# Performance work log

Hardware: AMD Instinct MI355X
Metric: run time of the kernel (lower is better)

The kernel has to match this reference:

```python
import jax, jax.numpy as jnp
import numpy as np

B, C, H, W = 4, 64, 64, 64
CQK = C // 4  # query/key channels = in_dim // 4


def setup_inputs() -> dict:
    key = jax.random.key(0)
    ks = jax.random.split(key, 9)
    s = 0.05
    return {
        "x": jax.random.normal(ks[0], (B, C, H, W), jnp.float32),
        "x_RGB": jax.random.normal(ks[1], (B, C, H, W), jnp.float32),
        "Wq": jax.random.normal(ks[2], (CQK, C), jnp.float32) * s,  # 1x1 conv weight
        "bq": jax.random.normal(ks[3], (CQK,), jnp.float32) * s,
        "Wk": jax.random.normal(ks[4], (CQK, C), jnp.float32) * s,
        "bk": jax.random.normal(ks[5], (CQK,), jnp.float32) * s,
        "Wv": jax.random.normal(ks[6], (C, C), jnp.float32) * s,
        "bv": jax.random.normal(ks[7], (C,), jnp.float32) * s,
        "lam": jnp.zeros((1,), jnp.float32) + 0.5,  # nn.Parameter init is 0; use 0.5 so output depends on attention
    }


def reference(x, x_RGB, Wq, bq, Wk, bk, Wv, bv, lam):
    b, c, h, w = x.shape
    n = h * w
    xf = x.reshape(b, c, n)          # B,C,N
    xr = x_RGB.reshape(b, c, n)      # B,C,N
    # 1x1 convs are channel matmuls
    q = jnp.einsum('oc,bcn->bno', Wq, xr) + bq            # B,N,Cqk  (permuted query)
    k = jnp.einsum('oc,bcn->bon', Wk, xf) + bk[:, None]   # B,Cqk,N
    v = jnp.einsum('oc,bcn->bon', Wv, xf) + bv[:, None]   # B,C,N
    energy = jnp.einsum('bio,boj->bij', q, k)             # B,N,N
    attention = jax.nn.softmax(energy, axis=-1)
    # out[b,c,i] = sum_j V[b,c,j] * attention[b,i,j]
    out = jnp.einsum('bcj,bij->bci', v, attention)        # B,C,N
    out = out.reshape(b, c, h, w)
    return lam[0] * out + x
```

## Files before the change

### kernel.cpp

```cpp
#include <hip/hip_runtime.h>
#include <hip/hip_bf16.h>
#include <math.h>

#define B_   4
#define C_   64
#define N_   4096
#define L2E  1.4426950408889634f

typedef __attribute__((ext_vector_type(8)))  short bf16x8;
typedef __attribute__((ext_vector_type(4)))  float f32x4;
typedef __attribute__((ext_vector_type(16))) float f32x16;
typedef __attribute__((ext_vector_type(4)))  uint  uint4v;

#define MFMA16(a,b,c) __builtin_amdgcn_mfma_f32_16x16x32_bf16(a,b,c,0,0,0)
#define MFMA32(a,b,c) __builtin_amdgcn_mfma_f32_32x32x16_bf16(a,b,c,0,0,0)

static __device__ inline uint cvtpk(float lo, float hi) {
    uint r;
    asm("v_cvt_pk_bf16_f32 %0, %1, %2" : "=v"(r) : "v"(lo), "v"(hi));
    return r;
}
static __device__ inline void plswap(uint &a, uint &b) {
    asm("v_permlane32_swap_b32 %0, %1" : "+v"(a), "+v"(b));
}
static __device__ inline float ex2(float x) {
#if __has_builtin(__builtin_amdgcn_exp2f)
    return __builtin_amdgcn_exp2f(x);
#else
    return exp2f(x);
#endif
}
static __device__ inline float frcp(float x) {
#if __has_builtin(__builtin_amdgcn_rcpf)
    return __builtin_amdgcn_rcpf(x);
#else
    return 1.0f / x;
#endif
}
static __device__ inline float tsum16(const f32x16 &s) {
    float a0 = s[0] + s[1],  a1 = s[2] + s[3];
    float a2 = s[4] + s[5],  a3 = s[6] + s[7];
    float a4 = s[8] + s[9],  a5 = s[10] + s[11];
    float a6 = s[12] + s[13], a7 = s[14] + s[15];
    a0 += a1; a2 += a3; a4 += a5; a6 += a7;
    return (a0 + a2) + (a4 + a6);
}
static __device__ inline bf16x8 pk8(float f0, float f1, float f2, float f3,
                                    float f4, float f5, float f6, float f7) {
    uint4v u = {cvtpk(f0, f1), cvtpk(f2, f3), cvtpk(f4, f5), cvtpk(f6, f7)};
    return __builtin_bit_cast(bf16x8, u);
}

__global__ __launch_bounds__(256) void qkv_mfma(
    const float* __restrict__ x, const float* __restrict__ xrgb,
    const float* __restrict__ Wq, const float* __restrict__ bq,
    const float* __restrict__ Wk, const float* __restrict__ bk,
    const float* __restrict__ Wv, const float* __restrict__ bv,
    ushort* __restrict__ Qo, ushort* __restrict__ Ko, ushort* __restrict__ Vo)
{
    const int t = threadIdx.x, b = blockIdx.y, n0 = blockIdx.x * 32;
    const int w = t >> 6, lane = t & 63, li = lane & 15, g = lane >> 4;
    const int pw = w & 1, oh = w >> 1;

    const int px = n0 + pw * 16 + li;

    bf16x8 bxf[2], brf[2];
    #pragma unroll
    for (int kk = 0; kk < 2; ++kk) {
        const int c0 = kk * 32 + g * 8;
        const float* xb = x + ((size_t)b * C_ + c0) * N_ + px;
        float fx[8];
        #pragma unroll
        for (int r = 0; r < 8; ++r) fx[r] = xb[(size_t)r * N_];
        bxf[kk] = pk8(fx[0], fx[1], fx[2], fx[3], fx[4], fx[5], fx[6], fx[7]);
        if (oh == 0) {
            const float* rb = xrgb + ((size_t)b * C_ + c0) * N_ + px;
            float fr[8];
            #pragma unroll
            for (int r = 0; r < 8; ++r) fr[r] = rb[(size_t)r * N_];
            brf[kk] = pk8(fr[0], fr[1], fr[2], fr[3], fr[4], fr[5], fr[6], fr[7]);
        } else {
            brf[kk] = bxf[kk];
        }
    }

    const f32x4 cz = {0.f, 0.f, 0.f, 0.f};
    #pragma unroll
    for (int j = 0; j < 3; ++j) {
        const int ot = oh * 3 + j;
        const float* wsrc;
        const float* bsrc;
        if (ot == 0)      { wsrc = Wq + li * 64;                   bsrc = bq; }
        else if (ot == 1) { wsrc = Wk + li * 64;                   bsrc = bk; }
        else              { wsrc = Wv + ((ot - 2) * 16 + li) * 64; bsrc = bv + (ot - 2) * 16; }
        const float s = (ot == 0) ? L2E : 1.0f;

        f32x4 acc = cz;
        #pragma unroll
        for (int kk = 0; kk < 2; ++kk) {
            const int c0 = kk * 32 + g * 8;
            const float4 a  = *(const float4*)(wsrc + c0);
            const float4 c4 = *(const float4*)(wsrc + c0 + 4);
            const bf16x8 wa = pk8(a.x * s, a.y * s, a.z * s, a.w * s,
                                  c4.x * s, c4.y * s, c4.z * s, c4.w * s);
            acc = MFMA16(wa, (ot == 0 ? brf[kk] : bxf[kk]), acc);
        }
        const float b0 = bsrc[g * 4 + 0] * s, b1 = bsrc[g * 4 + 1] * s;
        const float b2 = bsrc[g * 4 + 2] * s, b3 = bsrc[g * 4 + 3] * s;
        if (ot < 2) {
            uint2 pwd;
            pwd.x = cvtpk(acc[0] + b0, acc[1] + b1);
            pwd.y = cvtpk(acc[2] + b2, acc[3] + b3);
            ushort* dst = (ot == 0 ? Qo : Ko) + (size_t)(b * N_ + px) * 16 + g * 4;
            *(uint2*)dst = pwd;
        } else {
            const size_t base = (((size_t)b * (N_ / 16) + (px >> 4)) * 64
                                 + (ot - 2) * 16 + g * 4) * 16 + (px & 15);
            const uint v01 = cvtpk(acc[0] + b0, acc[1] + b1);
            const uint v23 = cvtpk(acc[2] + b2, acc[3] + b3);
            Vo[base]      = (ushort)(v01 & 0xffff);
            Vo[base + 16] = (ushort)(v01 >> 16);
            Vo[base + 32] = (ushort)(v23 & 0xffff);
            Vo[base + 48] = (ushort)(v23 >> 16);
        }
    }
}

__global__ __launch_bounds__(1024, 4) void flash32(
    const ushort* __restrict__ Qg, const ushort* __restrict__ Kg,
    const ushort* __restrict__ VT, const float* __restrict__ x,
    const float* __restrict__ lam, float* __restrict__ out)
{
    __shared__ float OT[16][64][33];
    __shared__ float LC[16][33];

    const int t = threadIdx.x, w = t >> 6, lane = t & 63;
    const int l31 = lane & 31, h = lane >> 5;
    const int qh = w & 1, jg = w >> 1;

    const int wg = blockIdx.x;
    const int b  = wg >> 6;
    const int i0 = (wg & 63) * 64;

    const bf16x8 qf = *(const bf16x8*)(Qg + ((size_t)(b * N_ + i0 + qh * 32 + l31)) * 16 + h * 8);

    const size_t jbase = (size_t)jg * 512;
    const ushort* kp = Kg + ((size_t)(b * N_) + jbase + l31) * 16 + h * 8;
    const ushort* vt = VT + (((size_t)b * (N_ / 16) + jg * 32) * 64 + l31) * 16 + h * 8;

    f32x16 a0, a1, z16;
    #pragma unroll
    for (int i = 0; i < 16; ++i) { a0[i] = 0.f; a1[i] = 0.f; z16[i] = 0.f; }
    float lsum = 0.f;

    #pragma unroll 1
    for (int jt = 0; jt < 16; ++jt) {
        const bf16x8 kf = *(const bf16x8*)(kp + (size_t)jt * 512);

        f32x16 st = MFMA32(kf, qf, z16);
        #pragma unroll
        for (int i = 0; i < 16; ++i) st[i] = ex2(st[i]);
        lsum += tsum16(st);

        uint A0 = cvtpk(st[0],  st[1]),  A1 = cvtpk(st[2],  st[3]);
        uint B0 = cvtpk(st[4],  st[5]),  B1 = cvtpk(st[6],  st[7]);
        uint C0 = cvtpk(st[8],  st[9]),  C1 = cvtpk(st[10], st[11]);
        uint D0 = cvtpk(st[12], st[13]), D1 = cvtpk(st[14], st[15]);
        plswap(A0, B0); plswap(A1, B1); plswap(C0, D0); plswap(C1, D1);
        uint4v u0 = {A0, A1, B0, B1}, u1 = {C0, C1, D0, D1};
        const bf16x8 pf0 = __builtin_bit_cast(bf16x8, u0);
        const bf16x8 pf1 = __builtin_bit_cast(bf16x8, u1);

        const ushort* vtj = vt + (size_t)jt * 2048;
        {
            const bf16x8 va = *(const bf16x8*)(vtj);
            const bf16x8 vb = *(const bf16x8*)(vtj + 512);
            a0 = MFMA32(va, pf0, a0);
            a1 = MFMA32(vb, pf0, a1);
        }
        {
            const bf16x8 va = *(const bf16x8*)(vtj + 1024);
            const bf16x8 vb = *(const bf16x8*)(vtj + 1536);
            a0 = MFMA32(va, pf1, a0);
            a1 = MFMA32(vb, pf1, a1);
        }
    }

    lsum += __shfl_xor(lsum, 32);
    if (h == 0) LC[w][l31] = lsum;

    #pragma unroll
    for (int r = 0; r < 16; ++r) {
        const int c = (r & 3) + 8 * (r >> 2) + 4 * h;
        OT[w][c][l31]      = a0[r];
        OT[w][c + 32][l31] = a1[r];
    }
    __syncthreads();

    {
        const int qh2 = t >> 9, c = (t >> 3) & 63, q0 = (t & 7) * 4;
        const float la = lam[0];
        f32x4 o = {0.f, 0.f, 0.f, 0.f};
        f32x4 ls = {0.f, 0.f, 0.f, 0.f};
        #pragma unroll
        for (int p = 0; p < 8; ++p) {
            const int idx = p * 2 + qh2;
            const f32x4 v = *(const f32x4*)&OT[idx][c][q0];
            o[0] += v[0]; o[1] += v[1]; o[2] += v[2]; o[3] += v[3];
            #pragma unroll
            for (int k = 0; k < 4; ++k) ls[k] += LC[idx][q0 + k];
        }
        const size_t off = ((size_t)b * C_ + c) * N_ + i0 + qh2 * 32 + q0;
        const float4 xv = *(const float4*)(x + off);
        float4 res;
        res.x = la * o[0] * frcp(ls[0]) + xv.x;
        res.y = la * o[1] * frcp(ls[1]) + xv.y;
        res.z = la * o[2] * frcp(ls[2]) + xv.z;
        res.w = la * o[3] * frcp(ls[3]) + xv.w;
        *(float4*)(out + off) = res;
    }
}

extern "C" void kernel_launch(void* const* d_in, const int* in_sizes, int n_in,
                              void* d_out, int out_size, void* d_ws, size_t ws_size,
                              hipStream_t stream)
{
    (void)in_sizes; (void)n_in; (void)out_size; (void)ws_size;
    const float* x    = (const float*)d_in[0];
    const float* xrgb = (const float*)d_in[1];
    const float* Wq   = (const float*)d_in[2];
    const float* bq   = (const float*)d_in[3];
    const float* Wk   = (const float*)d_in[4];
    const float* bk   = (const float*)d_in[5];
    const float* Wv   = (const float*)d_in[6];
    const float* bv   = (const float*)d_in[7];
    const float* lam  = (const float*)d_in[8];
    float* out = (float*)d_out;

    ushort* Qw = (ushort*)d_ws;
    ushort* Kw = Qw + (size_t)B_ * N_ * 16;
    ushort* Vw = Kw + (size_t)B_ * N_ * 16;

    qkv_mfma<<<dim3(N_ / 32, B_), 256, 0, stream>>>(
        x, xrgb, Wq, bq, Wk, bk, Wv, bv, Qw, Kw, Vw);

    flash32<<<dim3(256), 1024, 0, stream>>>(
        Qw, Kw, Vw, x, lam, out);
}
```

Before: 30.53 us.

## Process both query halves per wave to reuse K/V loads across queries

Measured after the change: 32.58 us. +6.7%, slower.

```diff
diff --git a/kernel.cpp b/kernel.cpp
--- a/kernel.cpp
+++ b/kernel.cpp
@@ -49,6 +49,16 @@
                                     float f4, float f5, float f6, float f7) {
     uint4v u = {cvtpk(f0, f1), cvtpk(f2, f3), cvtpk(f4, f5), cvtpk(f6, f7)};
     return __builtin_bit_cast(bf16x8, u);
+}
+static __device__ inline void pack_p(const f32x16 &st, bf16x8 &pf0, bf16x8 &pf1) {
+    uint A0 = cvtpk(st[0],  st[1]),  A1 = cvtpk(st[2],  st[3]);
+    uint B0 = cvtpk(st[4],  st[5]),  B1 = cvtpk(st[6],  st[7]);
+    uint C0 = cvtpk(st[8],  st[9]),  C1 = cvtpk(st[10], st[11]);
+    uint D0 = cvtpk(st[12], st[13]), D1 = cvtpk(st[14], st[15]);
+    plswap(A0, B0); plswap(A1, B1); plswap(C0, D0); plswap(C1, D1);
+    uint4v u0 = {A0, A1, B0, B1}, u1 = {C0, C1, D0, D1};
+    pf0 = __builtin_bit_cast(bf16x8, u0);
+    pf1 = __builtin_bit_cast(bf16x8, u1);
 }
 
 __global__ __launch_bounds__(256) void qkv_mfma(
@@ -61,7 +71,6 @@
     const int t = threadIdx.x, b = blockIdx.y, n0 = blockIdx.x * 32;
     const int w = t >> 6, lane = t & 63, li = lane & 15, g = lane >> 4;
     const int pw = w & 1, oh = w >> 1;
-
     const int px = n0 + pw * 16 + li;
 
     bf16x8 bxf[2], brf[2];
@@ -132,92 +141,115 @@
     const float* __restrict__ lam, float* __restrict__ out)
 {
     __shared__ float OT[16][64][33];
-    __shared__ float LC[16][33];
+    __shared__ float LC[2][16][33];
 
     const int t = threadIdx.x, w = t >> 6, lane = t & 63;
     const int l31 = lane & 31, h = lane >> 5;
-    const int qh = w & 1, jg = w >> 1;
 
     const int wg = blockIdx.x;
     const int b  = wg >> 6;
     const int i0 = (wg & 63) * 64;
 
-    const bf16x8 qf = *(const bf16x8*)(Qg + ((size_t)(b * N_ + i0 + qh * 32 + l31)) * 16 + h * 8);
-
-    const size_t jbase = (size_t)jg * 512;
+    const bf16x8 qfA = *(const bf16x8*)(Qg + ((size_t)(b * N_ + i0 + l31)) * 16 + h * 8);
+    const bf16x8 qfB = *(const bf16x8*)(Qg + ((size_t)(b * N_ + i0 + 32 + l31)) * 16 + h * 8);
+
+    const size_t jbase = (size_t)w * 256;
     const ushort* kp = Kg + ((size_t)(b * N_) + jbase + l31) * 16 + h * 8;
-    const ushort* vt = VT + (((size_t)b * (N_ / 16) + jg * 32) * 64 + l31) * 16 + h * 8;
-
-    f32x16 a0, a1, z16;
-    #pragma unroll
-    for (int i = 0; i < 16; ++i) { a0[i] = 0.f; a1[i] = 0.f; z16[i] = 0.f; }
-    float lsum = 0.f;
+    const ushort* vt = VT + (((size_t)b * (N_ / 16) + w * 16) * 64 + l31) * 16 + h * 8;
+
+    f32x16 aA0, aA1, aB0, aB1, z16;
+    #pragma unroll
+    for (int i = 0; i < 16; ++i) {
+        aA0[i] = 0.f; aA1[i] = 0.f; aB0[i] = 0.f; aB1[i] = 0.f; z16[i] = 0.f;
+    }
+    float lA = 0.f, lB = 0.f;
 
     #pragma unroll 1
-    for (int jt = 0; jt < 16; ++jt) {
+    for (int jt = 0; jt < 8; ++jt) {
         const bf16x8 kf = *(const bf16x8*)(kp + (size_t)jt * 512);
-
-        f32x16 st = MFMA32(kf, qf, z16);
-        #pragma unroll
-        for (int i = 0; i < 16; ++i) st[i] = ex2(st[i]);
-        lsum += tsum16(st);
-
-        uint A0 = cvtpk(st[0],  st[1]),  A1 = cvtpk(st[2],  st[3]);
-        uint B0 = cvtpk(st[4],  st[5]),  B1 = cvtpk(st[6],  st[7]);
-        uint C0 = cvtpk(st[8],  st[9]),  C1 = cvtpk(st[10], st[11]);
-        uint D0 = cvtpk(st[12], st[13]), D1 = cvtpk(st[14], st[15]);
-        plswap(A0, B0); plswap(A1, B1); plswap(C0, D0); plswap(C1, D1);
-        uint4v u0 = {A0, A1, B0, B1}, u1 = {C0, C1, D0, D1};
-        const bf16x8 pf0 = __builtin_bit_cast(bf16x8, u0);
-        const bf16x8 pf1 = __builtin_bit_cast(bf16x8, u1);
-
         const ushort* vtj = vt + (size_t)jt * 2048;
+        const bf16x8 va0 = *(const bf16x8*)(vtj);
+        const bf16x8 vb0 = *(const bf16x8*)(vtj + 512);
+        const bf16x8 va1 = *(const bf16x8*)(vtj + 1024);
+        const bf16x8 vb1 = *(const bf16x8*)(vtj + 1536);
+
         {
-            const bf16x8 va = *(const bf16x8*)(vtj);
-            const bf16x8 vb = *(const bf16x8*)(vtj + 512);
-            a0 = MFMA32(va, pf0, a0);
-            a1 = MFMA32(vb, pf0, a1);
+            f32x16 st = MFMA32(kf, qfA, z16);
+            #pragma unroll
+            for (int i = 0; i < 16; ++i) st[i] = ex2(st[i]);
+            lA += tsum16(st);
+            bf16x8 pf0, pf1;
+            pack_p(st, pf0, pf1);
+            aA0 = MFMA32(va0, pf0, aA0);
+            aA1 = MFMA32(vb0, pf0, aA1);
+            aA0 = MFMA32(va1, pf1, aA0);
+            aA1 = MFMA32(vb1, pf1, aA1);
         }
         {
-            const bf16x8 va = *(const bf16x8*)(vtj + 1024);
-            const bf16x8 vb = *(const bf16x8*)(vtj + 1536);
-            a0 = MFMA32(va, pf1, a0);
-            a1 = MFMA32(vb, pf1, a1);
-        }
-    }
-
-    lsum += __shfl_xor(lsum, 32);
-    if (h == 0) LC[w][l31] = lsum;
+            f32x16 st = MFMA32(kf, qfB, z16);
+            #pragma unroll
+            for (int i = 0; i < 16; ++i) st[i] = ex2(st[i]);
+            lB += tsum16(st);
+            bf16x8 pf0, pf1;
+            pack_p(st, pf0, pf1);
+            aB0 = MFMA32(va0, pf0, aB0);
+            aB1 = MFMA32(vb0, pf0, aB1);
+            aB0 = MFMA32(va1, pf1, aB0);
+            aB1 = MFMA32(vb1, pf1, aB1);
+        }
+    }
+
+    lA += __shfl_xor(lA, 32);
+    lB += __shfl_xor(lB, 32);
+    if (h == 0) { LC[0][w][l31] = lA; LC[1][w][l31] = lB; }
+
+    const float la = lam[0];
 
     #pragma unroll
     for (int r = 0; r < 16; ++r) {
         const int c = (r & 3) + 8 * (r >> 2) + 4 * h;
-        OT[w][c][l31]      = a0[r];
-        OT[w][c + 32][l31] = a1[r];
+        OT[w][c][l31]      = aA0[r];
+        OT[w][c + 32][l31] = aA1[r];
     }
     __syncthreads();
-
     {
-        const int qh2 = t >> 9, c = (t >> 3) & 63, q0 = (t & 7) * 4;
-        const float la = lam[0];
-        f32x4 o = {0.f, 0.f, 0.f, 0.f};
-        f32x4 ls = {0.f, 0.f, 0.f, 0.f};
-        #pragma unroll
-        for (int p = 0; p < 8; ++p) {
-            const int idx = p * 2 + qh2;
-            const f32x4 v = *(const f32x4*)&OT[idx][c][q0];
-            o[0] += v[0]; o[1] += v[1]; o[2] += v[2]; o[3] += v[3];
-            #pragma unroll
-            for (int k = 0; k < 4; ++k) ls[k] += LC[idx][q0 + k];
-        }
-        const size_t off = ((size_t)b * C_ + c) * N_ + i0 + qh2 * 32 + q0;
-        const float4 xv = *(const float4*)(x + off);
-        float4 res;
-        res.x = la * o[0] * frcp(ls[0]) + xv.x;
-        res.y = la * o[1] * frcp(ls[1]) + xv.y;
-        res.z = la * o[2] * frcp(ls[2]) + xv.z;
-        res.w = la * o[3] * frcp(ls[3]) + xv.w;
-        *(float4*)(out + off) = res;
+        const int c = t >> 4, qd = (t & 15) * 2;
+        float o0 = 0.f, o1 = 0.f, l0 = 0.f, l1 = 0.f;
+        #pragma unroll
+        for (int p = 0; p < 16; ++p) {
+            o0 += OT[p][c][qd];     o1 += OT[p][c][qd + 1];
+            l0 += LC[0][p][qd];     l1 += LC[0][p][qd + 1];
+        }
+        const size_t off = ((size_t)b * C_ + c) * N_ + i0 + qd;
+        const float2 xv = *(const float2*)(x + off);
+        float2 res;
+        res.x = la * o0 * frcp(l0) + xv.x;
+        res.y = la * o1 * frcp(l1) + xv.y;
+        *(float2*)(out + off) = res;
+    }
+    __syncthreads();
+
+    #pragma unroll
+    for (int r = 0; r < 16; ++r) {
+        const int c = (r & 3) + 8 * (r >> 2) + 4 * h;
+        OT[w][c][l31]      = aB0[r];
+        OT[w][c + 32][l31] = aB1[r];
+    }
+    __syncthreads();
+    {
+        const int c = t >> 4, qd = (t & 15) * 2;
+        float o0 = 0.f, o1 = 0.f, l0 = 0.f, l1 = 0.f;
+        #pragma unroll
+        for (int p = 0; p < 16; ++p) {
+            o0 += OT[p][c][qd];     o1 += OT[p][c][qd + 1];
+            l0 += LC[1][p][qd];     l1 += LC[1][p][qd + 1];
+        }
+        const size_t off = ((size_t)b * C_ + c) * N_ + i0 + 32 + qd;
+        const float2 xv = *(const float2*)(x + off);
+        float2 res;
+        res.x = la * o0 * frcp(l0) + xv.x;
+        res.y = la * o1 * frcp(l1) + xv.y;
+        *(float2*)(out + off) = res;
     }
 }
 
```
